# Kernel optimization log

Measured on AMD Instinct MI355X. Metric: run time of the kernel, lower is better.

The kernel has to match this reference:

```python
import jax, jax.numpy as jnp
import numpy as np

B, T, N, C = 4, 12, 200, 64
ATT = 128      # hard-coded attention_dim in GCN_OPERATION
H = 64         # AdjGen LSTM hidden size
DA = 64        # AdjGen adjacency projection dim
OUT_F = 128    # num_of_out_features
PRED = 12      # predict_length
NFILT = 3      # len(filters) per STSGCM
DATA_LEN = T - 4  # after 2 STSGCL layers


def setup_inputs() -> dict:
    key = jax.random.key(0)
    ks = jax.random.split(key, 16)
    s = 0.05
    f32 = jnp.float32
    return {
        "x": jax.random.normal(ks[0], (B, T, N, C), f32),
        "cur_epi": 5,
        "his_hn": jax.random.normal(ks[1], (B, H), f32),
        "his_cn": jax.random.normal(ks[2], (B, H), f32),
        "Wqkv": jax.random.normal(ks[3], (C, 3 * ATT), f32) * s,
        "bqkv": jnp.zeros((3 * ATT,), f32),
        "Wlin": jax.random.normal(ks[4], (ATT, C), f32) * s,
        "blin": jnp.zeros((C,), f32),
        "Wa": jax.random.normal(ks[5], (C, DA), f32) * s,
        "Wb": jax.random.normal(ks[6], (C, DA), f32) * s,
        "Wx_lstm": jax.random.normal(ks[7], (C, 4 * H), f32) * s,
        "Wh_lstm": jax.random.normal(ks[8], (H, 4 * H), f32) * s,
        "b_lstm": jnp.zeros((4 * H,), f32),
        "temb0": jax.random.normal(ks[9], (1, T, 1, C), f32) * 0.01,
        "temb1": jax.random.normal(ks[10], (1, T - 2, 1, C), f32) * 0.01,
        "semb": jax.random.normal(ks[11], (1, 1, N, C), f32) * 0.01,
        "Wo": jax.random.normal(ks[12], (DATA_LEN * C, OUT_F), f32) * s,
        "bo": jnp.zeros((OUT_F,), f32),
    }


def _forward(x, his_hn, his_cn, Wqkv, bqkv, Wlin, blin, Wa, Wb,
             Wx_lstm, Wh_lstm, b_lstm, temb0, temb1, semb, Wo, bo):
    dt = x.dtype
    att_scale = jnp.sqrt(jnp.asarray(float(ATT), dt))
    adj_scale = jnp.sqrt(jnp.asarray(float(DA), dt))

    def adjgen(xw):
        # xw: (B, nw, M, C). Stand-in for AdjGen (source unavailable):
        # content-dependent learned adjacency over M=3N nodes + one LSTM step.
        node = xw.mean(axis=(0, 1))                                  # (M, C)
        logits = (node @ Wa) @ (node @ Wb).T / adj_scale             # (M, M)
        adj = jax.nn.sigmoid(logits)
        pooled = xw.mean(axis=(1, 2))                                # (B, C)
        gates = pooled @ Wx_lstm + his_hn @ Wh_lstm + b_lstm
        i, f, g, o = jnp.split(gates, 4, axis=-1)
        c_n = jax.nn.sigmoid(f) * his_cn + jax.nn.sigmoid(i) * jnp.tanh(g)
        h_n = jax.nn.sigmoid(o) * jnp.tanh(c_n)
        return adj, logits, h_n, c_n

    def gcn_op(xw, adj):
        # QK^T softmax attention rescaled by adj, renormalized, then AV.
        Bn, nw, M, Cc = xw.shape
        xf = xw.reshape(Bn * nw, M, Cc)
        qkv = xf @ Wqkv + bqkv
        q, k, v = jnp.split(qkv, 3, axis=-1)                          # (BW, M, ATT)
        scores = jnp.einsum('bmd,bnd->bmn', q, k) / att_scale         # (BW, M, M)
        aw = jax.nn.softmax(scores, axis=-1) * adj
        ssum = aw.sum(-1, keepdims=True)
        mask = (ssum > 0).astype(dt)
        w = aw / (ssum + 1e-8) * mask
        out = jnp.einsum('bmn,bnd->bmd', w, jax.nn.relu(v)) @ Wlin + blin
        return out.reshape(Bn, nw, M, -1)

    def stsgcm(xw, Nn):
        cands = []
        cur = xw
        hn = cn = None
        for _ in range(NFILT):
            adj, _logits, hn, cn = adjgen(cur)
            cur = gcn_op(cur, adj)
            Bn, nw, M, F = cur.shape
            # keep only the middle-window copy of the N vertices: [2N:3N]
            cands.append(cur.reshape(Bn * nw, M, F)[:, 2 * Nn:3 * Nn, :])
        out = jnp.max(jnp.stack(cands, axis=0), axis=0)               # (B*nw, N, F)
        return out, hn, cn

    def stsgcl(xw, temb):
        Bn, Tt, Nn, Cc = xw.shape
        xw = xw + temb + semb                                         # position embedding
        nw = Tt - 2
        idx = jnp.arange(nw)[:, None] + jnp.arange(3)[None, :]        # (nw, 3)
        t_all = xw[:, idx].reshape(Bn, nw, 3 * Nn, Cc)
        out, hn, cn = stsgcm(t_all, Nn)
        return out.reshape(Bn, nw, Nn, -1), hn, cn

    h, hn, cn = stsgcl(x, temb0)
    h, hn, cn = stsgcl(h, temb1)
    # OUTPUT layer: (B, T', N, F) -> (B, N, T'*F) -> ReLU(Linear) -> tile PRED times on dim 1
    Bn, Tt, Nn, F = h.shape
    d = h.transpose(0, 2, 1, 3).reshape(Bn, Nn, Tt * F)
    o1 = jax.nn.relu(d @ Wo + bo)                                     # (B, N, OUT_F)
    return jnp.tile(o1, (1, PRED, 1))                                 # (B, PRED*N, OUT_F)


def reference(x, cur_epi, his_hn, his_cn, Wqkv, bqkv, Wlin, blin, Wa, Wb,
              Wx_lstm, Wh_lstm, b_lstm, temb0, temb1, semb, Wo, bo):
    del cur_epi  # annealing schedule of the (unavailable) AdjGen; unused here
    return _forward(x, his_hn, his_cn, Wqkv, bqkv, Wlin, blin, Wa, Wb,
                    Wx_lstm, Wh_lstm, b_lstm, temb0, temb1, semb, Wo, bo)
```

## Files before the change

### kernel.cpp

```cpp
#include <hip/hip_runtime.h>
#include <hip/hip_bf16.h>
#include <math.h>

constexpr int Bc   = 4;
constexpr int Nc   = 200;
constexpr int Cc   = 64;
constexpr int Mc   = 600;
constexpr int ATTc = 128;
constexpr int OUTFc = 128;
constexpr int PREDc = 12;
constexpr int MAXBW = 40;
constexpr int MPAD  = 640;

typedef short short4v __attribute__((ext_vector_type(4)));
typedef short short8 __attribute__((ext_vector_type(8)));
typedef float f32x4  __attribute__((ext_vector_type(4)));

static __device__ __forceinline__ void bsplit(float v, short& h, short& l) {
    __hip_bfloat16 hb = __float2bfloat16(v);
    float hf = __bfloat162float(hb);
    __hip_bfloat16 lb = __float2bfloat16(v - hf);
    h = *(short*)&hb; l = *(short*)&lb;
}

__global__ __launch_bounds__(256)
void embed_window_k(const float* __restrict__ src, const float* __restrict__ temb,
                    const float* __restrict__ semb, float* __restrict__ dst,
                    int Tin, int nw, long total)
{
    long idx = (long)blockIdx.x * 256 + threadIdx.x;
    if (idx >= total) return;
    int c = (int)(idx & 63);
    long r = idx >> 6;
    int n = (int)(r % Nc); r /= Nc;
    int j = (int)(r % 3);  r /= 3;
    int w = (int)(r % nw);
    int b = (int)(r / nw);
    int t = w + j;
    dst[idx] = src[(((long)b * Tin + t) * Nc + n) * Cc + c]
             + temb[t * Cc + c] + semb[n * Cc + c];
}

__global__ __launch_bounds__(256)
void mean_nab_k(const float* __restrict__ cur, const float* __restrict__ Wa,
                const float* __restrict__ Wb,
                ushort* __restrict__ NAH, ushort* __restrict__ NAL,
                ushort* __restrict__ NBH, ushort* __restrict__ NBL, int BW)
{
    __shared__ float Ns[64][17];
    __shared__ float Ws[64][132];
    const int m0 = blockIdx.x * 16;
    const int t = threadIdx.x;
    for (int e = t; e < 1024; e += 256) {
        int r = e >> 4, c4 = (e & 15) << 2;
        *(float4*)&Ws[r][c4]      = *(const float4*)&Wa[r * 64 + c4];
        *(float4*)&Ws[r][64 + c4] = *(const float4*)&Wb[r * 64 + c4];
    }
    {
        int row = t >> 4, c4 = (t & 15) << 2;
        int gm = m0 + row;
        float4 sv = make_float4(0.f, 0.f, 0.f, 0.f);
        if (gm < Mc) {
            for (int bw = 0; bw < BW; bw++) {
                const float4 v = *(const float4*)&cur[((long)bw * Mc + gm) * Cc + c4];
                sv.x += v.x; sv.y += v.y; sv.z += v.z; sv.w += v.w;
            }
        }
        const float inv = 1.f / BW;
        Ns[c4 + 0][row] = sv.x * inv; Ns[c4 + 1][row] = sv.y * inv;
        Ns[c4 + 2][row] = sv.z * inv; Ns[c4 + 3][row] = sv.w * inv;
    }
    __syncthreads();
    const int row = t >> 4, c8 = (t & 15) * 8;
    float acc[8] = {};
    for (int k = 0; k < 64; k++) {
        float a = Ns[k][row];
        float b[8];
        *(float4*)&b[0] = *(const float4*)&Ws[k][c8];
        *(float4*)&b[4] = *(const float4*)&Ws[k][c8 + 4];
#pragma unroll
        for (int j = 0; j < 8; j++) acc[j] += a * b[j];
    }
    int gm = m0 + row;
    if (gm < Mc) {
#pragma unroll
        for (int j = 0; j < 8; j++) {
            int col = c8 + j;
            short h, l;
            bsplit(acc[j], h, l);
            if (col < 64) { NAH[gm * 64 + col] = (ushort)h; NAL[gm * 64 + col] = (ushort)l; }
            else { NBH[gm * 64 + col - 64] = (ushort)h; NBL[gm * 64 + col - 64] = (ushort)l; }
        }
    }
}

__global__ __launch_bounds__(256)
void prep_k(const float* __restrict__ Wlin,
            ushort* __restrict__ WTH, ushort* __restrict__ WTL,
            const float* __restrict__ Wqkv,
            ushort* __restrict__ WQH, ushort* __restrict__ WQL)
{
    int i = blockIdx.x * 256 + threadIdx.x;
    if (i < 64 * 128) {
        int c = i >> 7, a = i & 127;
        short h, l;
        bsplit(Wlin[a * 64 + c], h, l);
        WTH[c * 128 + a] = (ushort)h;
        WTL[c * 128 + a] = (ushort)l;
    } else {
        int j = i - 64 * 128;
        if (j < 384 * 64) {
            int n = j >> 6, c = j & 63;
            short h, l;
            bsplit(Wqkv[c * 384 + n], h, l);
            WQH[n * 64 + c] = (ushort)h;
            WQL[n * 64 + c] = (ushort)l;
        }
    }
}

__global__ __launch_bounds__(256)
void qkv_adj_k(const float* __restrict__ CURp,
               const ushort* __restrict__ WQH, const ushort* __restrict__ WQL,
               const float* __restrict__ bias,
               ushort* __restrict__ QH, ushort* __restrict__ QL,
               ushort* __restrict__ KH, ushort* __restrict__ KL,
               ushort* __restrict__ VTH, ushort* __restrict__ VTL,
               const ushort* __restrict__ Ah, const ushort* __restrict__ Al,
               const ushort* __restrict__ Bh, const ushort* __restrict__ Bl,
               float* __restrict__ ADJ, int nqkv)
{
    __shared__ __align__(16) ushort SM[36864];
    const int t = threadIdx.x;
    const int lane = t & 63, w = t >> 6;
    const int lm = lane & 15, lq = lane >> 4;

    if ((int)blockIdx.x >= nqkv) {
        const int b2 = blockIdx.x - nqkv;
        const int m0 = (b2 / 5) * 128, n0 = (b2 % 5) * 128;
        ushort (*As)[128][40] = (ushort (*)[128][40])(SM);
        ushort (*Bs)[128][40] = (ushort (*)[128][40])(SM + 10240);
        const int wm = (w >> 1) * 64, wn = (w & 1) * 64;

        f32x4 acc[4][4];
#pragma unroll
        for (int i = 0; i < 4; i++)
#pragma unroll
            for (int j = 0; j < 4; j++)
#pragma unroll
                for (int r = 0; r < 4; r++) acc[i][j][r] = 0.f;

        for (int k0 = 0; k0 < 64; k0 += 32) {
            __syncthreads();
#pragma unroll
            for (int p = 0; p < 2; p++) {
                int e = t + p * 256;
                int row = e >> 2, ks = (e & 3) << 3;
                {
                    int gm = m0 + row;
                    short8 vh, vl;
#pragma unroll
                    for (int q = 0; q < 8; q++) { vh[q] = 0; vl[q] = 0; }
                    if (gm < Mc) {
                        vh = *(const short8*)(Ah + (long)gm * 64 + k0 + ks);
                        vl = *(const short8*)(Al + (long)gm * 64 + k0 + ks);
                    }
                    *(short8*)&As[0][row][ks] = vh;
                    *(short8*)&As[1][row][ks] = vl;
                }
                {
                    int gn = n0 + row;
                    short8 vh, vl;
#pragma unroll
                    for (int q = 0; q < 8; q++) { vh[q] = 0; vl[q] = 0; }
                    if (gn < Mc) {
                        vh = *(const short8*)(Bh + (long)gn * 64 + k0 + ks);
                        vl = *(const short8*)(Bl + (long)gn * 64 + k0 + ks);
                    }
                    *(short8*)&Bs[0][row][ks] = vh;
                    *(short8*)&Bs[1][row][ks] = vl;
                }
            }
            __syncthreads();

            short8 af[4][2], bf[4][2];
#pragma unroll
            for (int i = 0; i < 4; i++) {
                af[i][0] = *(const short8*)&As[0][wm + i * 16 + lm][lq * 8];
                af[i][1] = *(const short8*)&As[1][wm + i * 16 + lm][lq * 8];
            }
#pragma unroll
            for (int j = 0; j < 4; j++) {
                bf[j][0] = *(const short8*)&Bs[0][wn + j * 16 + lm][lq * 8];
                bf[j][1] = *(const short8*)&Bs[1][wn + j * 16 + lm][lq * 8];
            }
#pragma unroll
            for (int i = 0; i < 4; i++)
#pragma unroll
                for (int j = 0; j < 4; j++) {
                    acc[i][j] = __builtin_amdgcn_mfma_f32_16x16x32_bf16(af[i][0], bf[j][0], acc[i][j], 0, 0, 0);
                    acc[i][j] = __builtin_amdgcn_mfma_f32_16x16x32_bf16(af[i][0], bf[j][1], acc[i][j], 0, 0, 0);
                    acc[i][j] = __builtin_amdgcn_mfma_f32_16x16x32_bf16(af[i][1], bf[j][0], acc[i][j], 0, 0, 0);
                }
        }
#pragma unroll
        for (int i = 0; i < 4; i++) {
            int gmb = m0 + wm + i * 16 + lq * 4;
#pragma unroll
            for (int j = 0; j < 4; j++) {
                int gn = n0 + wn + j * 16 + lm;
                if (gn >= Mc) continue;
#pragma unroll
                for (int r = 0; r < 4; r++) {
                    int gm = gmb + r;
                    if (gm < Mc)
                        ADJ[(long)gm * Mc + gn] = 1.f / (1.f + __expf(-acc[i][j][r] * 0.125f));
                }
            }
        }
        return;
    }

    ushort* AsH = SM;
    ushort* AsL = SM + 9216;
    ushort* BsH = SM + 18432;
    ushort* BsL = SM + 27648;
    const int bid = blockIdx.x;
    const int xcd = bid & 7, slot = bid >> 3;
    const int z = (slot / 15) * 8 + xcd;
    const int r15 = slot % 15;
    const int which = r15 % 3;
    const int m0 = (r15 / 3) * 128;
    const int nb = which * 128;
    const float* A = CURp + (long)z * Mc * Cc;
    const int wm = (w >> 1) * 64, wn = (w & 1) * 64;

#pragma unroll
    for (int p = 0; p < 8; p++) {
        int e = t + p * 256;
        int row = e >> 4, k4 = (e & 15) * 4;
        int gm = m0 + row;
        float4 v = make_float4(0.f, 0.f, 0.f, 0.f);
        if (gm < Mc) v = *(const float4*)(A + (long)gm * 64 + k4);
        short4v h4, l4;
        short hs, ls;
        bsplit(v.x, hs, ls); h4[0] = hs; l4[0] = ls;
        bsplit(v.y, hs, ls); h4[1] = hs; l4[1] = ls;
        bsplit(v.z, hs, ls); h4[2] = hs; l4[2] = ls;
        bsplit(v.w, hs, ls); h4[3] = hs; l4[3] = ls;
        *(short4v*)(AsH + row * 72 + k4) = h4;
        *(short4v*)(AsL + row * 72 + k4) = l4;
    }
#pragma unroll
    for (int p = 0; p < 4; p++) {
        int e = t + p * 256;
        int row = e >> 3, seg = (e & 7) * 8;
        *(short8*)(BsH + row * 72 + seg) = *(const short8*)(WQH + (long)(nb + row) * 64 + seg);
        *(short8*)(BsL + row * 72 + seg) = *(const short8*)(WQL + (long)(nb + row) * 64 + seg);
    }
    __syncthreads();

    f32x4 acc[4][4];
#pragma unroll
    for (int i = 0; i < 4; i++)
#pragma unroll
        for (int j = 0; j < 4; j++)
#pragma unroll
            for (int r = 0; r < 4; r++) acc[i][j][r] = 0.f;

#pragma unroll
    for (int ks = 0; ks < 2; ks++) {
        short8 af[4][2], bf[4][2];
#pragma unroll
        for (int i = 0; i < 4; i++) {
            af[i][0] = *(const short8*)(AsH + (wm + i * 16 + lm) * 72 + ks * 32 + lq * 8);
            af[i][1] = *(const short8*)(AsL + (wm + i * 16 + lm) * 72 + ks * 32 + lq * 8);
        }
#pragma unroll
        for (int j = 0; j < 4; j++) {
            bf[j][0] = *(const short8*)(BsH + (wn + j * 16 + lm) * 72 + ks * 32 + lq * 8);
            bf[j][1] = *(const short8*)(BsL + (wn + j * 16 + lm) * 72 + ks * 32 + lq * 8);
        }
#pragma unroll
        for (int i = 0; i < 4; i++)
#pragma unroll
            for (int j = 0; j < 4; j++) {
                acc[i][j] = __builtin_amdgcn_mfma_f32_16x16x32_bf16(af[i][0], bf[j][0], acc[i][j], 0, 0, 0);
                acc[i][j] = __builtin_amdgcn_mfma_f32_16x16x32_bf16(af[i][0], bf[j][1], acc[i][j], 0, 0, 0);
                acc[i][j] = __builtin_amdgcn_mfma_f32_16x16x32_bf16(af[i][1], bf[j][0], acc[i][j], 0, 0, 0);
            }
    }
    __syncthreads();

    uint* CP = (uint*)SM;
#pragma unroll
    for (int i = 0; i < 4; i++)
#pragma unroll
        for (int j = 0; j < 4; j++) {
            int col = wn + j * 16 + lm;
            float b = bias[nb + col];
#pragma unroll
            for (int r = 0; r < 4; r++) {
                int row = wm + i * 16 + lq * 4 + r;
                float v = acc[i][j][r] + b;
                if (which == 2) v = fmaxf(v, 0.f);
                short hs, ls;
                bsplit(v, hs, ls);
                CP[row * 132 + col] = ((uint)(ushort)ls << 16) | (uint)(ushort)hs;
            }
        }
    __syncthreads();

    if (which == 2) {
        ushort* vh = VTH + (long)z * ATTc * MPAD;
        ushort* vl = VTL + (long)z * ATTc * MPAD;
#pragma unroll
        for (int p = 0; p < 8; p++) {
            int e = t + p * 256;
            int col = e >> 4, rg = (e & 15) * 8;
            if (m0 + rg < Mc) {
                short8 h8, l8;
#pragma unroll
                for (int q = 0; q < 8; q++) {
                    uint u = CP[(rg + q) * 132 + col];
                    h8[q] = (short)(u & 0xffff);
                    l8[q] = (short)(u >> 16);
                }
                *(short8*)(vh + (long)col * MPAD + m0 + rg) = h8;
                *(short8*)(vl + (long)col * MPAD + m0 + rg) = l8;
            }
        }
    } else {
        ushort* dh = (which == 0 ? QH : KH) + (long)z * Mc * ATTc;
        ushort* dl = (which == 0 ? QL : KL) + (long)z * Mc * ATTc;
#pragma unroll
        for (int p = 0; p < 8; p++) {
            int e = t + p * 256;
            int row = e >> 4, seg = (e & 15) * 8;
            int gm = m0 + row;
            if (gm < Mc) {
                short8 h8, l8;
#pragma unroll
                for (int q = 0; q < 8; q++) {
                    uint u = CP[row * 132 + seg + q];
                    h8[q] = (short)(u & 0xffff);
                    l8[q] = (short)(u >> 16);
                }
                *(short8*)(dh + (long)gm * ATTc + seg) = h8;
                *(short8*)(dl + (long)gm * ATTc + seg) = l8;
            }
        }
    }
}

#define ISSUE_K(Dh, Dl, kc_, g_)                                        \
  _Pragma("unroll")                                                     \
  for (int p = 0; p < 4; p++) {                                         \
    int key = (kc_) + srow0 + 32 * p;                                   \
    short8 vh, vl;                                                      \
    _Pragma("unroll")                                                   \
    for (int q2 = 0; q2 < 8; q2++) { vh[q2] = 0; vl[q2] = 0; }          \
    if (key < Mc) {                                                     \
      vh = *(const short8*)(Khz + (long)key * ATTc + (g_) * 64 + sks);  \
      vl = *(const short8*)(Klz + (long)key * ATTc + (g_) * 64 + sks);  \
    }                                                                   \
    Dh[p] = vh; Dl[p] = vl;                                             \
  }

#define ISSUE_V(Dh, Dl, kc_, g_)                                                   \
  _Pragma("unroll")                                                                \
  for (int p = 0; p < 4; p++) {                                                    \
    int att = srow0 + 32 * p;                                                      \
    Dh[p] = *(const short8*)(Vhz + (long)att * MPAD + (kc_) + (g_) * 64 + sks);    \
    Dl[p] = *(const short8*)(Vlz + (long)att * MPAD + (kc_) + (g_) * 64 + sks);    \
  }

#define WRITE_SB(Dh, Dl)                                                \
  _Pragma("unroll")                                                     \
  for (int p = 0; p < 4; p++) {                                         \
    *(short8*)&SB[0][srow0 + 32 * p][sks] = Dh[p];                      \
    *(short8*)&SB[1][srow0 + 32 * p][sks] = Dl[p];                      \
  }

#define MFMA_QK(base_)                                                   \
  _Pragma("unroll")                                                      \
  for (int kk = 0; kk < 2; kk++) {                                       \
    _Pragma("unroll")                                                    \
    for (int j = 0; j < 8; j++) {                                        \
      short8 bh = *(const short8*)&SB[0][j * 16 + lm][kk * 32 + lq * 8]; \
      short8 bl = *(const short8*)&SB[1][j * 16 + lm][kk * 32 + lq * 8]; \
      sacc[j] = __builtin_amdgcn_mfma_f32_16x16x32_bf16(qh[(base_) + kk], bh, sacc[j], 0, 0, 0); \
      sacc[j] = __builtin_amdgcn_mfma_f32_16x16x32_bf16(qh[(base_) + kk], bl, sacc[j], 0, 0, 0); \
      sacc[j] = __builtin_amdgcn_mfma_f32_16x16x32_bf16(ql[(base_) + kk], bh, sacc[j], 0, 0, 0); \
    }                                                                    \
  }

#define MFMA_PV(g_)                                                      \
  _Pragma("unroll")                                                      \
  for (int kk = 0; kk < 2; kk++) {                                       \
    int po = ((g_) * 64 + kk * 32 + lq * 8) ^ ((lm >> 2) << 3);          \
    short8 ph = *(const short8*)&PH[w][lm][po];                          \
    short8 pl = *(const short8*)&PL[w][lm][po];                          \
    _Pragma("unroll")                                                    \
    for (int j = 0; j < 8; j++) {                                        \
      short8 vh = *(const short8*)&SB[0][j * 16 + lm][kk * 32 + lq * 8]; \
      short8 vl = *(const short8*)&SB[1][j * 16 + lm][kk * 32 + lq * 8]; \
      oacc[j] = __builtin_amdgcn_mfma_f32_16x16x32_bf16(ph, vh, oacc[j], 0, 0, 0); \
      oacc[j] = __builtin_amdgcn_mfma_f32_16x16x32_bf16(ph, vl, oacc[j], 0, 0, 0); \
      oacc[j] = __builtin_amdgcn_mfma_f32_16x16x32_bf16(pl, vh, oacc[j], 0, 0, 0); \
    }                                                                    \
  }

__global__ __launch_bounds__(256, 2)
void attn_k(const ushort* __restrict__ QH, const ushort* __restrict__ QL,
            const ushort* __restrict__ KH, const ushort* __restrict__ KL,
            const ushort* __restrict__ VTH, const ushort* __restrict__ VTL,
            const float* __restrict__ adj,
            const ushort* __restrict__ WTH, const ushort* __restrict__ WTL,
            const float* __restrict__ blin,
            float* __restrict__ CUR, float* __restrict__ cand, int first,
            float scale)
{
    __shared__ __align__(16) ushort SMEM[37888];
    typedef ushort sb_t[128][72];
    typedef ushort ph_t[16][152];
    sb_t* SB = (sb_t*)SMEM;
    ph_t* PH = (ph_t*)(SMEM + 18432);
    ph_t* PL = (ph_t*)(SMEM + 28160);
    const int bid = blockIdx.x;
    const int xcd = bid & 7, slot = bid >> 3;
    const int z = (slot / 10) * 8 + xcd;
    const int m0 = (slot % 10) * 64;
    const int t = threadIdx.x;
    const int lane = t & 63, w = t >> 6;
    const int lm = lane & 15, lq = lane >> 4;
    const int qrow0 = m0 + w * 16;
    const int srow0 = t >> 3;
    const int sks   = (t & 7) << 3;

    const ushort* Qhz = QH + (long)z * Mc * ATTc;
    const ushort* Qlz = QL + (long)z * Mc * ATTc;
    const ushort* Khz = KH + (long)z * Mc * ATTc;
    const ushort* Klz = KL + (long)z * Mc * ATTc;
    const ushort* Vhz = VTH + (long)z * ATTc * MPAD;
    const ushort* Vlz = VTL + (long)z * ATTc * MPAD;

    short8 RAh[4], RAl[4], RBh[4], RBl[4];
    ISSUE_K(RAh, RAl, 0, 0);

    short8 qh[4], ql[4];
    {
        int qr = qrow0 + lm;
        if (qr < Mc) {
            const ushort* qp = Qhz + (long)qr * ATTc;
            const ushort* qp2 = Qlz + (long)qr * ATTc;
#pragma unroll
            for (int ks = 0; ks < 4; ks++) {
                qh[ks] = *(const short8*)(qp + ks * 32 + lq * 8);
                ql[ks] = *(const short8*)(qp2 + ks * 32 + lq * 8);
            }
        } else {
#pragma unroll
            for (int ks = 0; ks < 4; ks++)
#pragma unroll
                for (int q = 0; q < 8; q++) { qh[ks][q] = 0; ql[ks][q] = 0; }
        }
    }

    f32x4 oacc[8];
#pragma unroll
    for (int j = 0; j < 8; j++)
#pragma unroll
        for (int r = 0; r < 4; r++) oacc[j][r] = 0.f;
    float Er[4] = {}, Sr[4] = {};
    float adjv[8][4];

    for (int c = 0; c < 5; c++) {
        const int kc = c * 128;
        f32x4 sacc[8];
#pragma unroll
        for (int j = 0; j < 8; j++)
#pragma unroll
            for (int r = 0; r < 4; r++) sacc[j][r] = 0.f;

        __syncthreads();
        WRITE_SB(RAh, RAl);
        ISSUE_K(RBh, RBl, kc, 1);
#pragma unroll
        for (int j = 0; j < 8; j++) {
            int col = kc + j * 16 + lm;
#pragma unroll
            for (int r = 0; r < 4; r++) {
                int row = qrow0 + lq * 4 + r;
                adjv[j][r] = (col < Mc && row < Mc) ? adj[(long)row * Mc + col] : 0.f;
            }
        }
        __syncthreads();
        MFMA_QK(0);

        __syncthreads();
        WRITE_SB(RBh, RBl);
        ISSUE_V(RAh, RAl, kc, 0);
        __syncthreads();
        MFMA_QK(2);

#pragma unroll
        for (int j = 0; j < 8; j++) {
            int col = kc + j * 16 + lm;
            bool cok = col < Mc;
#pragma unroll
            for (int r = 0; r < 4; r++) {
                float e = cok ? __expf(sacc[j][r] * scale) : 0.f;
                float p = e * adjv[j][r];
                Er[r] += e; Sr[r] += p;
                short hs, ls;
                bsplit(p, hs, ls);
                int cs = (j * 16 + lm) ^ (lq << 3);
                PH[w][lq * 4 + r][cs] = (ushort)hs;
                PL[w][lq * 4 + r][cs] = (ushort)ls;
            }
        }

        __syncthreads();
        WRITE_SB(RAh, RAl);
        ISSUE_V(RBh, RBl, kc, 1);
        __syncthreads();
        MFMA_PV(0);

        __syncthreads();
        WRITE_SB(RBh, RBl);
        if (c < 4) { ISSUE_K(RAh, RAl, kc + 128, 0); }
        __syncthreads();
        MFMA_PV(1);
    }

#pragma unroll
    for (int mk = 1; mk <= 8; mk <<= 1)
#pragma unroll
        for (int r = 0; r < 4; r++) {
            Er[r] += __shfl_xor(Er[r], mk, 64);
            Sr[r] += __shfl_xor(Sr[r], mk, 64);
        }
    float inv[4];
#pragma unroll
    for (int r = 0; r < 4; r++) inv[r] = 1.f / (Sr[r] + 1e-8f * Er[r]);

    __syncthreads();
    uint*   OP  = (uint*)SMEM;
    ushort* BsF = SMEM + 16896;

#pragma unroll
    for (int p = 0; p < 4; p++) {
        int e = t + p * 256;
        int row = e >> 4, seg = (e & 15) << 3;
        *(short8*)(BsF + row * 136 + seg) = *(const short8*)(WTH + row * 128 + seg);
        *(short8*)(BsF + 64 * 136 + row * 136 + seg) = *(const short8*)(WTL + row * 128 + seg);
    }
#pragma unroll
    for (int j = 0; j < 8; j++)
#pragma unroll
        for (int r = 0; r < 4; r++) {
            int lrow = w * 16 + lq * 4 + r;
            float v = oacc[j][r] * inv[r];
            short hs, ls;
            bsplit(v, hs, ls);
            OP[lrow * 132 + j * 16 + lm] = ((uint)(ushort)ls << 16) | (uint)(ushort)hs;
        }
    __syncthreads();

    f32x4 cacc[4];
#pragma unroll
    for (int jj = 0; jj < 4; jj++)
#pragma unroll
        for (int r = 0; r < 4; r++) cacc[jj][r] = 0.f;

#pragma unroll
    for (int ks = 0; ks < 4; ks++) {
        short8 ah, al;
        {
            const uint* src = OP + (w * 16 + lm) * 132 + ks * 32 + lq * 8;
            const uint4 u0 = *(const uint4*)src;
            const uint4 u1 = *(const uint4*)(src + 4);
#pragma unroll
            for (int q = 0; q < 4; q++) {
                uint u = ((const uint*)&u0)[q];
                ah[q] = (short)(u & 0xffff); al[q] = (short)(u >> 16);
            }
#pragma unroll
            for (int q = 0; q < 4; q++) {
                uint u = ((const uint*)&u1)[q];
                ah[4 + q] = (short)(u & 0xffff); al[4 + q] = (short)(u >> 16);
            }
        }
#pragma unroll
        for (int jj = 0; jj < 4; jj++) {
            short8 bh = *(const short8*)(BsF + (jj * 16 + lm) * 136 + ks * 32 + lq * 8);
            short8 bl = *(const short8*)(BsF + 64 * 136 + (jj * 16 + lm) * 136 + ks * 32 + lq * 8);
            cacc[jj] = __builtin_amdgcn_mfma_f32_16x16x32_bf16(ah, bh, cacc[jj], 0, 0, 0);
            cacc[jj] = __builtin_amdgcn_mfma_f32_16x16x32_bf16(ah, bl, cacc[jj], 0, 0, 0);
            cacc[jj] = __builtin_amdgcn_mfma_f32_16x16x32_bf16(al, bh, cacc[jj], 0, 0, 0);
        }
    }

    float* CURz = CUR + (long)z * Mc * Cc;
#pragma unroll
    for (int jj = 0; jj < 4; jj++) {
        int col = jj * 16 + lm;
        float b = blin[col];
#pragma unroll
        for (int r = 0; r < 4; r++) {
            int row = m0 + w * 16 + lq * 4 + r;
            if (row < Mc) {
                float v = cacc[jj][r] + b;
                CURz[(long)row * Cc + col] = v;
                if (row >= 2 * Nc) {
                    long o = ((long)z * Nc + (row - 2 * Nc)) * Cc + col;
                    cand[o] = first ? v : fmaxf(cand[o], v);
                }
            }
        }
    }
}

#undef ISSUE_K
#undef ISSUE_V
#undef WRITE_SB
#undef MFMA_QK
#undef MFMA_PV

__global__ __launch_bounds__(128)
void output_k(const float* __restrict__ h2, const float* __restrict__ Wo,
              const float* __restrict__ bo, float* __restrict__ out)
{
    __shared__ float ds[512];
    int row = blockIdx.x;
    int b = row / Nc, n = row % Nc;
    int t = threadIdx.x;
    for (int e = t; e < 512; e += 128) {
        int tt = e >> 6, c = e & 63;
        ds[e] = h2[(((long)b * 8 + tt) * Nc + n) * Cc + c];
    }
    __syncthreads();
    float acc = bo[t];
    for (int e = 0; e < 512; e++) acc += ds[e] * Wo[e * OUTFc + t];
    acc = fmaxf(acc, 0.f);
    for (int p = 0; p < PREDc; p++)
        out[(((long)b * PREDc + p) * Nc + n) * (long)OUTFc + t] = acc;
}

extern "C" void kernel_launch(void* const* d_in, const int* in_sizes, int n_in,
                              void* d_out, int out_size, void* d_ws, size_t ws_size,
                              hipStream_t stream)
{
    (void)in_sizes; (void)n_in; (void)out_size; (void)ws_size;
    const float* x     = (const float*)d_in[0];
    const float* Wqkv  = (const float*)d_in[4];
    const float* bqkv  = (const float*)d_in[5];
    const float* Wlin  = (const float*)d_in[6];
    const float* blin  = (const float*)d_in[7];
    const float* Wa    = (const float*)d_in[8];
    const float* Wb    = (const float*)d_in[9];
    const float* temb0 = (const float*)d_in[13];
    const float* temb1 = (const float*)d_in[14];
    const float* semb  = (const float*)d_in[15];
    const float* Wo    = (const float*)d_in[16];
    const float* bo    = (const float*)d_in[17];
    float* out = (float*)d_out;

    float* ws   = (float*)d_ws;
    float* CUR  = ws;
    float* ADJ  = CUR + (long)MAXBW * Mc * Cc;
    float* CAND = ADJ + (long)Mc * Mc;
    uint*  OB   = (uint*)(CAND + (long)MAXBW * Nc * Cc);
    float* QHf  = (float*)(OB + (long)MAXBW * Mc * ATTc);
    const long QSZ = (long)MAXBW * Mc * ATTc / 2;
    float* QLf  = QHf + QSZ;
    float* KHf  = QLf + QSZ;
    float* KLf  = KHf + QSZ;
    float* VTHf = KLf + QSZ;
    float* VTLf = VTHf + (long)MAXBW * ATTc * MPAD / 2;
    ushort* NAH = (ushort*)(VTLf + (long)MAXBW * ATTc * MPAD / 2);
    ushort* NAL = NAH + Mc * Cc;
    ushort* NBH = NAL + Mc * Cc;
    ushort* NBL = NBH + Mc * Cc;
    ushort* WTH = NBL + Mc * Cc;
    ushort* WTL = WTH + 64 * 128;
    ushort* WQH = WTL + 64 * 128;
    ushort* WQL = WQH + 384 * 64;

    ushort* QH  = (ushort*)QHf;
    ushort* QL  = (ushort*)QLf;
    ushort* KH  = (ushort*)KHf;
    ushort* KL  = (ushort*)KLf;
    ushort* VTH = (ushort*)VTHf;
    ushort* VTL = (ushort*)VTLf;

    const float inv_sqrt_att = 0.08838834764831845f;

    prep_k<<<dim3(128), dim3(256), 0, stream>>>(Wlin, WTH, WTL, Wqkv, WQH, WQL);

    for (int layer = 0; layer < 2; layer++) {
        int Tin = layer ? 10 : 12;
        int nw  = Tin - 2;
        int BW  = Bc * nw;
        const float* src  = layer ? CAND : x;
        const float* temb = layer ? temb1 : temb0;

        long etotal = (long)BW * Mc * Cc;
        embed_window_k<<<dim3((unsigned)((etotal + 255) / 256)), dim3(256), 0, stream>>>(
            src, temb, semb, CUR, Tin, nw, etotal);

        for (int it = 0; it < 3; it++) {
            mean_nab_k<<<dim3(38), dim3(256), 0, stream>>>(
                CUR, Wa, Wb, NAH, NAL, NBH, NBL, BW);

            int nqkv = BW * 15;
            qkv_adj_k<<<dim3(nqkv + 25), dim3(256), 0, stream>>>(
                CUR, WQH, WQL, bqkv, QH, QL, KH, KL, VTH, VTL,
                NAH, NAL, NBH, NBL, ADJ, nqkv);

            attn_k<<<dim3(BW * 10), dim3(256), 0, stream>>>(
                QH, QL, KH, KL, VTH, VTL, ADJ, WTH, WTL, blin,
                CUR, CAND, it == 0 ? 1 : 0, inv_sqrt_att);
        }
    }
    output_k<<<dim3(Bc * Nc), dim3(128), 0, stream>>>(CAND, Wo, bo, out);
}
```

Baseline: 647.4 us.

## Spread node-mean projection over more blocks and prefetch Wlin in attention loop

The node-mean/projection kernel now handles 4 nodes per block instead of 16, with scalar coalesced loads and one output column per thread, and launches 150 blocks instead of 38. The goal is to fill more compute units in a latency-bound reduction. In the attention kernel, the final loop iteration (which has no next K tile to fetch) now loads the Wlin hi/lo tiles into the idle prefetch registers, so the epilogue writes them to shared memory from registers rather than from global memory. The cost is that Wa/Wb are reloaded into shared memory by four times as many blocks.

```diff
diff --git a/kernel.cpp b/kernel.cpp
--- a/kernel.cpp
+++ b/kernel.cpp
@@ -47,9 +47,9 @@
                 ushort* __restrict__ NAH, ushort* __restrict__ NAL,
                 ushort* __restrict__ NBH, ushort* __restrict__ NBL, int BW)
 {
-    __shared__ float Ns[64][17];
+    __shared__ float Ns[4][64];
     __shared__ float Ws[64][132];
-    const int m0 = blockIdx.x * 16;
+    const int m0 = blockIdx.x * 4;
     const int t = threadIdx.x;
     for (int e = t; e < 1024; e += 256) {
         int r = e >> 4, c4 = (e & 15) << 2;
@@ -57,40 +57,26 @@
         *(float4*)&Ws[r][64 + c4] = *(const float4*)&Wb[r * 64 + c4];
     }
     {
-        int row = t >> 4, c4 = (t & 15) << 2;
+        int row = t >> 6, c = t & 63;
         int gm = m0 + row;
-        float4 sv = make_float4(0.f, 0.f, 0.f, 0.f);
-        if (gm < Mc) {
-            for (int bw = 0; bw < BW; bw++) {
-                const float4 v = *(const float4*)&cur[((long)bw * Mc + gm) * Cc + c4];
-                sv.x += v.x; sv.y += v.y; sv.z += v.z; sv.w += v.w;
-            }
-        }
-        const float inv = 1.f / BW;
-        Ns[c4 + 0][row] = sv.x * inv; Ns[c4 + 1][row] = sv.y * inv;
-        Ns[c4 + 2][row] = sv.z * inv; Ns[c4 + 3][row] = sv.w * inv;
+        float sv = 0.f;
+        for (int bw = 0; bw < BW; bw++)
+            sv += cur[((long)bw * Mc + gm) * Cc + c];
+        Ns[row][c] = sv / BW;
     }
     __syncthreads();
-    const int row = t >> 4, c8 = (t & 15) * 8;
-    float acc[8] = {};
-    for (int k = 0; k < 64; k++) {
-        float a = Ns[k][row];
-        float b[8];
-        *(float4*)&b[0] = *(const float4*)&Ws[k][c8];
-        *(float4*)&b[4] = *(const float4*)&Ws[k][c8 + 4];
-#pragma unroll
-        for (int j = 0; j < 8; j++) acc[j] += a * b[j];
-    }
-    int gm = m0 + row;
-    if (gm < Mc) {
-#pragma unroll
-        for (int j = 0; j < 8; j++) {
-            int col = c8 + j;
-            short h, l;
-            bsplit(acc[j], h, l);
-            if (col < 64) { NAH[gm * 64 + col] = (ushort)h; NAL[gm * 64 + col] = (ushort)l; }
-            else { NBH[gm * 64 + col - 64] = (ushort)h; NBL[gm * 64 + col - 64] = (ushort)l; }
-        }
+#pragma unroll
+    for (int o = 0; o < 2; o++) {
+        int e = t + o * 256;
+        int row = e >> 7, col = e & 127;
+        float acc = 0.f;
+        for (int k = 0; k < 64; k++)
+            acc += Ns[row][k] * Ws[k][col];
+        int gm = m0 + row;
+        short h, l;
+        bsplit(acc, h, l);
+        if (col < 64) { NAH[gm * 64 + col] = (ushort)h; NAL[gm * 64 + col] = (ushort)l; }
+        else { NBH[gm * 64 + col - 64] = (ushort)h; NBL[gm * 64 + col - 64] = (ushort)l; }
     }
 }
 
@@ -529,7 +515,17 @@
 
         __syncthreads();
         WRITE_SB(RBh, RBl);
-        if (c < 4) { ISSUE_K(RAh, RAl, kc + 128, 0); }
+        if (c < 4) {
+            ISSUE_K(RAh, RAl, kc + 128, 0);
+        } else {
+#pragma unroll
+            for (int p = 0; p < 4; p++) {
+                int e = t + p * 256;
+                int row = e >> 4, seg = (e & 15) << 3;
+                RAh[p] = *(const short8*)(WTH + row * 128 + seg);
+                RAl[p] = *(const short8*)(WTL + row * 128 + seg);
+            }
+        }
         __syncthreads();
         MFMA_PV(1);
     }
@@ -553,8 +549,8 @@
     for (int p = 0; p < 4; p++) {
         int e = t + p * 256;
         int row = e >> 4, seg = (e & 15) << 3;
-        *(short8*)(BsF + row * 136 + seg) = *(const short8*)(WTH + row * 128 + seg);
-        *(short8*)(BsF + 64 * 136 + row * 136 + seg) = *(const short8*)(WTL + row * 128 + seg);
+        *(short8*)(BsF + row * 136 + seg) = RAh[p];
+        *(short8*)(BsF + 64 * 136 + row * 136 + seg) = RAl[p];
     }
 #pragma unroll
     for (int j = 0; j < 8; j++)
@@ -711,7 +707,7 @@
             src, temb, semb, CUR, Tin, nw, etotal);
 
         for (int it = 0; it < 3; it++) {
-            mean_nab_k<<<dim3(38), dim3(256), 0, stream>>>(
+            mean_nab_k<<<dim3(150), dim3(256), 0, stream>>>(
                 CUR, Wa, Wb, NAH, NAL, NBH, NBL, BW);
 
             int nqkv = BW * 15;
```

Measured after the change: 631.1 us. 2.5% less time.
